# Kernel tuning notes

Measured on AMD Instinct MI355X. Metric: run time of the kernel, lower is better.

## Reference

```python
import jax, jax.numpy as jnp
import numpy as np

FORGET_BIAS = 1.0  # TF LSTMCell default


def setup_inputs() -> dict:
    key = jax.random.key(0)
    k1, k2 = jax.random.split(key)
    B, T, D, H = 32, 512, 1024, 1024
    x = jax.random.normal(k1, (B, T, D), dtype=jnp.float32)
    sl = jax.random.randint(jax.random.fold_in(key, 1), (B,), 0, T, dtype=jnp.int32)
    # TF LSTMCell kernel: [D + H, 4H], gates ordered (i, j, f, o)
    kernel = jax.random.normal(k2, (D + H, 4 * H), dtype=jnp.float32) * 0.02
    bias = jnp.zeros((4 * H,), dtype=jnp.float32)
    return {"x": x, "sl": sl, "kernel": kernel, "bias": bias}


def reference(x, sl, kernel, bias):
    # x: [B, T, D]; process timesteps in REVERSED order (reverse=True in source).
    # Collect the cell state c (state[0] of LSTMStateTuple) at each step.
    B, T, D = x.shape
    H = kernel.shape[1] // 4

    xs = jnp.swapaxes(x[:, ::-1, :], 0, 1)  # [T, B, D], reversed time

    def step(carry, x_t):
        c, h = carry
        z = jnp.concatenate([x_t, h], axis=-1) @ kernel + bias  # [B, 4H]
        i, j, f, o = jnp.split(z, 4, axis=-1)
        c_new = jax.nn.sigmoid(f + FORGET_BIAS) * c + jax.nn.sigmoid(i) * jnp.tanh(j)
        h_new = jax.nn.sigmoid(o) * jnp.tanh(c_new)
        return (c_new, h_new), c_new

    c0 = jnp.zeros((B, H), dtype=x.dtype)
    h0 = jnp.zeros((B, H), dtype=x.dtype)
    _, cs = jax.lax.scan(step, (c0, h0), xs)  # [T, B, H] in processing order
    cell_states = jnp.swapaxes(cs, 0, 1)  # [B, T, H]
    return cell_states
```

## Files before the change

### kernel.cpp

```cpp
#include <hip/hip_runtime.h>
#include <cstdint>
#include <cstddef>

#define TLEN 512
#define HD   1024

typedef short bf16x8 __attribute__((ext_vector_type(8)));
typedef float f32x4  __attribute__((ext_vector_type(4)));

#define MFMA(a, b, c) __builtin_amdgcn_mfma_f32_16x16x32_bf16((a), (b), (c), 0, 0, 0)

static __device__ __forceinline__ unsigned short f2bf(float v) {
    unsigned u = __float_as_uint(v);
    u += 0x7fffu + ((u >> 16) & 1u);
    return (unsigned short)(u >> 16);
}
static __device__ __forceinline__ float bf2f(unsigned short s) {
    return __uint_as_float((unsigned)s << 16);
}

static __device__ __forceinline__ bf16x8 ld_h16a(const unsigned short* p) {
    bf16x8 r;
    asm volatile("global_load_dwordx4 %0, %1, off sc0 sc1"
                 : "=&v"(r) : "v"(p) : "memory");
    return r;
}

static __device__ __forceinline__ void st_bypass_u16(unsigned short* p, unsigned short v) {
    unsigned vv = v;
    asm volatile("global_store_short %0, %1, off sc0 sc1" :: "v"(p), "v"(vv) : "memory");
}
static __device__ __forceinline__ void st_bypass_u32(unsigned* p, unsigned v) {
    asm volatile("global_store_dword %0, %1, off sc0 sc1" :: "v"(p), "v"(v) : "memory");
}

__global__ __launch_bounds__(512, 2)
void lstm_persist(const float* __restrict__ x,
                  const float* __restrict__ W,
                  const float* __restrict__ bias,
                  float* __restrict__ out,
                  unsigned* __restrict__ slots,
                  unsigned short* __restrict__ hbase)
{
    const int tid  = threadIdx.x;
    const int cb   = blockIdx.x;
    const int bg   = cb >> 7;
    const int hcb  = cb & 127;
    const int wv   = tid >> 6;
    const int lane = tid & 63;
    const int mn   = lane & 15;
    const int q    = lane >> 4;

    __shared__ f32x4 red[8][2][64];
    __shared__ float zsh[16][33];
    __shared__ float cls[16][8];

    const int zc0 = ((mn >> 3)    ) * 1024 + hcb * 8 + (mn & 7);
    const int zc1 = ((mn >> 3) + 2) * 1024 + hcb * 8 + (mn & 7);
    const int kx0 = wv * 128;

    bf16x8 wxh[4][2], wxl[4][2], whh[4][2], whl[4][2];
    #pragma unroll
    for (int kk = 0; kk < 4; ++kk) {
        #pragma unroll
        for (int j = 0; j < 8; ++j) {
            const int r = kx0 + kk * 32 + q * 8 + j;
            float v0 = W[(size_t)r * 4096 + zc0];
            unsigned short h0 = f2bf(v0);
            wxh[kk][0][j] = (short)h0;
            wxl[kk][0][j] = (short)f2bf(v0 - bf2f(h0));
            float v1 = W[(size_t)r * 4096 + zc1];
            unsigned short h1 = f2bf(v1);
            wxh[kk][1][j] = (short)h1;
            wxl[kk][1][j] = (short)f2bf(v1 - bf2f(h1));
            float u0 = W[(size_t)(1024 + r) * 4096 + zc0];
            unsigned short g0 = f2bf(u0);
            whh[kk][0][j] = (short)g0;
            whl[kk][0][j] = (short)f2bf(u0 - bf2f(g0));
            float u1 = W[(size_t)(1024 + r) * 4096 + zc1];
            unsigned short g1 = f2bf(u1);
            whh[kk][1][j] = (short)g1;
            whl[kk][1][j] = (short)f2bf(u1 - bf2f(g1));
        }
    }

    float bi = 0.f, bj = 0.f, bff = 0.f, bo = 0.f;
    if (tid < 128) {
        int b = tid >> 3, hc = tid & 7;
        int c0 = hcb * 8 + hc;
        bi  = bias[c0];
        bj  = bias[1024 + c0];
        bff = bias[2048 + c0];
        bo  = bias[3072 + c0];
        cls[b][hc] = 0.f;
    }
    __syncthreads();

    f32x4 acc0 = {0.f, 0.f, 0.f, 0.f};
    f32x4 acc1 = {0.f, 0.f, 0.f, 0.f};

    auto do_xpart = [&](int tt) {
        const size_t b0 = ((size_t)(bg * 16 + mn) * TLEN + tt) * HD + kx0 + q * 8;
        #pragma unroll
        for (int kk = 0; kk < 4; ++kk) {
            const float* p0 = x + b0 + kk * 32;
            f32x4 a0 = *(const f32x4*)(p0);
            f32x4 a1 = *(const f32x4*)(p0 + 4);
            bf16x8 xh, xl;
            #pragma unroll
            for (int j = 0; j < 4; ++j) {
                float vv; unsigned short h;
                vv = a0[j]; h = f2bf(vv); xh[j]     = (short)h; xl[j]     = (short)f2bf(vv - bf2f(h));
                vv = a1[j]; h = f2bf(vv); xh[4 + j] = (short)h; xl[4 + j] = (short)f2bf(vv - bf2f(h));
            }
            acc0 = MFMA(xh, wxh[kk][0], acc0);
            acc0 = MFMA(xl, wxh[kk][0], acc0);
            acc0 = MFMA(xh, wxl[kk][0], acc0);
            acc1 = MFMA(xh, wxh[kk][1], acc1);
            acc1 = MFMA(xl, wxh[kk][1], acc1);
            acc1 = MFMA(xh, wxl[kk][1], acc1);
        }
    };

    auto do_hpart = [&](const unsigned short* Hh, const unsigned short* Hl) {
        const int off = (bg * 16 + mn) * HD + kx0 + q * 8;
        bf16x8 ah[4], al[4];
        #pragma unroll
        for (int kk = 0; kk < 4; ++kk) {
            ah[kk] = ld_h16a(Hh + off + kk * 32);
            al[kk] = ld_h16a(Hl + off + kk * 32);
        }
        asm volatile("s_waitcnt vmcnt(0)" ::: "memory");
        __builtin_amdgcn_sched_barrier(0);
        #pragma unroll
        for (int kk = 0; kk < 4; ++kk) {
            acc0 = MFMA(ah[kk], whh[kk][0], acc0);
            acc0 = MFMA(al[kk], whh[kk][0], acc0);
            acc0 = MFMA(ah[kk], whl[kk][0], acc0);
            acc1 = MFMA(ah[kk], whh[kk][1], acc1);
            acc1 = MFMA(al[kk], whh[kk][1], acc1);
            acc1 = MFMA(ah[kk], whl[kk][1], acc1);
        }
    };

    unsigned short* hhi0 = hbase;
    unsigned short* hlo0 = hbase + 32768;
    unsigned short* hhi1 = hbase + 65536;
    unsigned short* hlo1 = hbase + 98304;

    do_xpart(TLEN - 1);

    for (int t = 0; t < TLEN; ++t) {
        const unsigned short* Hh = (t & 1) ? hhi1 : hhi0;
        const unsigned short* Hl = (t & 1) ? hlo1 : hlo0;
        unsigned short* Ph = (t & 1) ? hhi0 : hhi1;
        unsigned short* Pl = (t & 1) ? hlo0 : hlo1;

        do_hpart(Hh, Hl);

        red[wv][0][lane] = acc0;
        red[wv][1][lane] = acc1;
        __syncthreads();
        if (tid < 128) {
            int frag = tid >> 6, l = tid & 63;
            f32x4 s = red[0][frag][l];
            #pragma unroll
            for (int w = 1; w < 8; ++w) s += red[w][frag][l];
            int nn = l & 15, qq = l >> 4;
            int m0 = qq * 4;
            zsh[m0 + 0][frag * 16 + nn] = s[0];
            zsh[m0 + 1][frag * 16 + nn] = s[1];
            zsh[m0 + 2][frag * 16 + nn] = s[2];
            zsh[m0 + 3][frag * 16 + nn] = s[3];
        }
        __syncthreads();
        if (tid < 128) {
            int b = tid >> 3, hc = tid & 7;
            float zi = zsh[b][hc]      + bi;
            float zj = zsh[b][8 + hc]  + bj;
            float zf = zsh[b][16 + hc] + bff;
            float zo = zsh[b][24 + hc] + bo;
            float co = cls[b][hc];
            float ig = 1.f / (1.f + expf(-zi));
            float fg = 1.f / (1.f + expf(-(zf + 1.0f)));
            float og = 1.f / (1.f + expf(-zo));
            float jt = tanhf(zj);
            float cn = fg * co + ig * jt;
            float hn = og * tanhf(cn);
            cls[b][hc] = cn;
            unsigned short hh = f2bf(hn);
            unsigned short hl = f2bf(hn - bf2f(hh));
            int wi = (bg * 16 + b) * HD + hcb * 8 + hc;
            st_bypass_u16(Ph + wi, hh);
            st_bypass_u16(Pl + wi, hl);
            __builtin_nontemporal_store(cn,
                &out[((size_t)(bg * 16 + b) * TLEN + t) * HD + hcb * 8 + hc]);
            asm volatile("s_waitcnt vmcnt(1)" ::: "memory");
        }
        acc0 = (f32x4){0.f, 0.f, 0.f, 0.f};
        acc1 = (f32x4){0.f, 0.f, 0.f, 0.f};
        __syncthreads();

        if (t + 1 < TLEN) {
            if (tid == 0) st_bypass_u32(&slots[cb], (unsigned)(t + 1));
            do_xpart(TLEN - 2 - t);
            if (wv < 4) {
                const unsigned tgt = (unsigned)(t + 1);
                const unsigned* sp = &slots[(wv << 6) + lane];
                while (__hip_atomic_load(sp, __ATOMIC_RELAXED,
                           __HIP_MEMORY_SCOPE_AGENT) < tgt) {
                    __builtin_amdgcn_s_sleep(1);
                }
            }
            __syncthreads();
        }
    }
}

extern "C" void kernel_launch(void* const* d_in, const int* in_sizes, int n_in,
                              void* d_out, int out_size, void* d_ws, size_t ws_size,
                              hipStream_t stream)
{
    (void)in_sizes; (void)n_in; (void)out_size; (void)ws_size;
    const float* x    = (const float*)d_in[0];
    const float* W    = (const float*)d_in[2];
    const float* bias = (const float*)d_in[3];
    float* out = (float*)d_out;

    unsigned* slots = (unsigned*)d_ws;
    unsigned short* hbase = (unsigned short*)((char*)d_ws + 4096);

    hipMemsetAsync(d_ws, 0, 4096 + 262144, stream);

    lstm_persist<<<256, 512, 0, stream>>>(x, W, bias, out, slots, hbase);
}
```

Measured before the change: 3.379 ms.

## Use per-XCC leader barrier and L2-cached hidden-state loads

Replaces the all-blocks polling barrier with a two-level scheme. The first block on each XCC becomes a leader: it polls every block's slot, then publishes a per-XCC flag, and the other blocks on that XCC spin only on that flag. Hidden-state loads drop the sc1 bit so they can be served from the XCC's L2; the leader issues an agent-scope acquire fence each step, meant to invalidate stale L2 lines before anyone reads the new h buffer. This cuts global polling traffic and h-load latency, but adds an extra hop to the barrier and relies on subtle cache-coherence ordering across XCCs.

Measured after the change: 3.502 ms. 3.7% more time.

```diff
diff --git a/kernel.cpp b/kernel.cpp
--- a/kernel.cpp
+++ b/kernel.cpp
@@ -19,9 +19,9 @@
     return __uint_as_float((unsigned)s << 16);
 }
 
-static __device__ __forceinline__ bf16x8 ld_h16a(const unsigned short* p) {
+static __device__ __forceinline__ bf16x8 ld_h16_l2(const unsigned short* p) {
     bf16x8 r;
-    asm volatile("global_load_dwordx4 %0, %1, off sc0 sc1"
+    asm volatile("global_load_dwordx4 %0, %1, off sc0"
                  : "=&v"(r) : "v"(p) : "memory");
     return r;
 }
@@ -54,6 +54,16 @@
     __shared__ f32x4 red[8][2][64];
     __shared__ float zsh[16][33];
     __shared__ float cls[16][8];
+    __shared__ int   sh_xcc, sh_leader;
+
+    if (tid == 0) {
+        unsigned xcc;
+        asm volatile("s_getreg_b32 %0, hwreg(HW_REG_XCC_ID, 0, 4)" : "=s"(xcc));
+        unsigned r = __hip_atomic_fetch_add(&slots[256 + xcc], 1u,
+                         __ATOMIC_RELAXED, __HIP_MEMORY_SCOPE_AGENT);
+        sh_xcc    = (int)xcc;
+        sh_leader = (r == 0u) ? 1 : 0;
+    }
 
     const int zc0 = ((mn >> 3)    ) * 1024 + hcb * 8 + (mn & 7);
     const int zc1 = ((mn >> 3) + 2) * 1024 + hcb * 8 + (mn & 7);
@@ -95,6 +105,8 @@
         cls[b][hc] = 0.f;
     }
     __syncthreads();
+    const bool leader = (sh_leader != 0);
+    unsigned* flagp = slots + 512 + sh_xcc * 16;
 
     f32x4 acc0 = {0.f, 0.f, 0.f, 0.f};
     f32x4 acc1 = {0.f, 0.f, 0.f, 0.f};
@@ -127,8 +139,8 @@
         bf16x8 ah[4], al[4];
         #pragma unroll
         for (int kk = 0; kk < 4; ++kk) {
-            ah[kk] = ld_h16a(Hh + off + kk * 32);
-            al[kk] = ld_h16a(Hl + off + kk * 32);
+            ah[kk] = ld_h16_l2(Hh + off + kk * 32);
+            al[kk] = ld_h16_l2(Hl + off + kk * 32);
         }
         asm volatile("s_waitcnt vmcnt(0)" ::: "memory");
         __builtin_amdgcn_sched_barrier(0);
@@ -202,14 +214,28 @@
         __syncthreads();
 
         if (t + 1 < TLEN) {
-            if (tid == 0) st_bypass_u32(&slots[cb], (unsigned)(t + 1));
+            const unsigned tgt = (unsigned)(t + 1);
+            if (tid == 0) {
+                st_bypass_u32(&slots[cb], tgt);
+                if (leader) __builtin_amdgcn_fence(__ATOMIC_ACQUIRE, "agent");
+            }
             do_xpart(TLEN - 2 - t);
-            if (wv < 4) {
-                const unsigned tgt = (unsigned)(t + 1);
-                const unsigned* sp = &slots[(wv << 6) + lane];
-                while (__hip_atomic_load(sp, __ATOMIC_RELAXED,
-                           __HIP_MEMORY_SCOPE_AGENT) < tgt) {
-                    __builtin_amdgcn_s_sleep(1);
+            if (leader) {
+                if (wv < 4) {
+                    const unsigned* sp = &slots[(wv << 6) + lane];
+                    while (__hip_atomic_load(sp, __ATOMIC_RELAXED,
+                               __HIP_MEMORY_SCOPE_AGENT) < tgt) {
+                        __builtin_amdgcn_s_sleep(1);
+                    }
+                }
+                __syncthreads();
+                if (tid == 0) st_bypass_u32(flagp, tgt);
+            } else {
+                if (tid == 0) {
+                    while (__hip_atomic_load(flagp, __ATOMIC_RELAXED,
+                               __HIP_MEMORY_SCOPE_AGENT) < tgt) {
+                        __builtin_amdgcn_s_sleep(1);
+                    }
                 }
             }
             __syncthreads();
```
